# Optimization experiments

Hardware: AMD Instinct MI355X
Metric: run time of the kernel (lower is better)

## Reference

```python
import jax, jax.numpy as jnp
import numpy as np

C = 256          # in_channels
CI = 128         # inter_channels = C // reduction
N_B, H, W = 4, 64, 64


def setup_inputs() -> dict:
    key = jax.random.key(0)
    ks = jax.random.split(key, 9)
    std = 0.01
    inp = {
        "x": jax.random.normal(ks[0], (N_B, C, H, W), dtype=jnp.float32),
        # 1x1 conv weights stored as [out_ch, in_ch]
        "w_g": jax.random.normal(ks[1], (CI, C), dtype=jnp.float32) * std,
        "b_g": jnp.zeros((CI,), dtype=jnp.float32),
        "w_theta": jax.random.normal(ks[2], (CI, C), dtype=jnp.float32) * std,
        "b_theta": jnp.zeros((CI,), dtype=jnp.float32),
        "w_phi": jax.random.normal(ks[3], (CI, C), dtype=jnp.float32) * std,
        "b_phi": jnp.zeros((CI,), dtype=jnp.float32),
        # conv_out: use small random instead of exact zeros so output is non-trivial
        "w_out": jax.random.normal(ks[4], (C, CI), dtype=jnp.float32) * std,
        "b_out": jnp.zeros((C,), dtype=jnp.float32),
    }
    return inp


def reference(x, w_g, b_g, w_theta, b_theta, w_phi, b_phi, w_out, b_out):
    n, c, h, w = x.shape
    nhw = h * w
    xf = x.reshape(n, c, nhw)                                   # [n, C, N]
    # 1x1 convs == channel matmuls
    g_x = jnp.einsum('ncs,oc->nso', xf, w_g) + b_g              # [n, N, CI]
    theta_x = jnp.einsum('ncs,oc->nso', xf, w_theta) + b_theta  # [n, N, CI]
    phi_x = jnp.einsum('ncs,oc->nos', xf, w_phi) + b_phi[None, :, None]  # [n, CI, N]
    # pairwise weights: [n, N, N]
    pw = jnp.einsum('nqc,ncs->nqs', theta_x, phi_x)
    # faithful to original: DIVIDE by d**-0.5 (i.e. multiply by sqrt(d))
    pw = pw / (theta_x.shape[-1] ** (-0.5))
    pw = jax.nn.softmax(pw, axis=-1)
    y = jnp.einsum('nqs,nsc->nqc', pw, g_x)                     # [n, N, CI]
    y = y.transpose(0, 2, 1).reshape(n, -1, h, w)               # [n, CI, H, W]
    out = jnp.einsum('nchw,oc->nohw', y, w_out) + b_out[None, :, None, None]
    return x + out
```

## Files before the change

kernel.cpp:

```cpp
#include <hip/hip_runtime.h>
#include <cmath>

typedef __attribute__((ext_vector_type(8))) short bf16x8;
typedef __attribute__((ext_vector_type(4))) float f32x4;

#define MFMA16(a,b,c) __builtin_amdgcn_mfma_f32_16x16x32_bf16((a),(b),(c),0,0,0)

#if __has_builtin(__builtin_amdgcn_exp2f)
#define EXP2F(x) __builtin_amdgcn_exp2f(x)
#else
#define EXP2F(x) exp2f(x)
#endif

#define KSCALE 16.3222312f
#define SMAX 44.0f

#define NB 4
#define CH 256
#define CI 128
#define NS 4096

__device__ __forceinline__ unsigned short f2bf(float f) {
    unsigned int u = __builtin_bit_cast(unsigned int, f);
    u += 0x7fffu + ((u >> 16) & 1u);
    return (unsigned short)(u >> 16);
}
__device__ __forceinline__ unsigned int pk2(float lo, float hi) {
    return (unsigned int)f2bf(lo) | ((unsigned int)f2bf(hi) << 16);
}
__device__ __forceinline__ unsigned int pk2t(float lo, float hi) {
    unsigned int ul = __builtin_bit_cast(unsigned int, lo);
    unsigned int uh = __builtin_bit_cast(unsigned int, hi);
    return (uh & 0xffff0000u) | (ul >> 16);
}

__device__ __forceinline__ void gload16(void* lds, const void* g) {
    __builtin_amdgcn_global_load_lds(
        (const __attribute__((address_space(1))) unsigned int*)g,
        (__attribute__((address_space(3))) unsigned int*)lds,
        16, 0, 0);
}

__global__ void wcvt_kernel(const float* __restrict__ w_g, const float* __restrict__ w_th,
                            const float* __restrict__ w_ph, const float* __restrict__ w_out,
                            const float* __restrict__ b_g, const float* __restrict__ b_th,
                            const float* __restrict__ b_ph,
                            unsigned short* __restrict__ wbf, float* __restrict__ bsc) {
    int i = blockIdx.x * 256 + threadIdx.x;
    float v;
    if (i < 32768)        v = w_g[i];
    else if (i < 65536)   v = w_th[i - 32768] * KSCALE;
    else if (i < 98304)   v = w_ph[i - 65536];
    else                  v = w_out[i - 98304];
    wbf[i] = f2bf(v);
    if (i < 128)          bsc[i] = b_g[i];
    else if (i < 256)     bsc[i] = b_th[i - 128] * KSCALE;
    else if (i < 384)     bsc[i] = b_ph[i - 256];
}

__global__ __launch_bounds__(256, 2)
void proj_kernel(const float* __restrict__ x,
                 const unsigned short* __restrict__ wbf, const float* __restrict__ bsc,
                 unsigned short* __restrict__ theta,
                 unsigned short* __restrict__ phi,
                 unsigned short* __restrict__ gT) {
    const int tid  = threadIdx.x;
    const int wid  = tid >> 6;
    const int lane = tid & 63;
    const int quad = lane >> 4;
    const int l15  = lane & 15;
    const int wi    = blockIdx.x;
    const int stile = blockIdx.y;
    const int n     = blockIdx.z;
    const int s0    = stile * 128;

    const float* xN = x + (size_t)n * CH * NS;
    const unsigned short* W = wbf + (size_t)wi * 32768;
    const float* Bv = bsc + wi * 128;

    __shared__ unsigned int xp[128 * 68];

    f32x4 acc[8][2];
#pragma unroll
    for (int ot = 0; ot < 8; ot++)
#pragma unroll
        for (int st = 0; st < 2; st++) acc[ot][st] = (f32x4){0.f, 0.f, 0.f, 0.f};

    for (int ch = 0; ch < 2; ch++) {
        __syncthreads();
#pragma unroll
        for (int i = 0; i < 8; i++) {
            int t  = tid + 256 * i;
            int cp = t >> 5;
            int s4 = t & 31;
            int c0 = ch * 128 + cp * 2;
            const float* p0 = xN + (size_t)c0 * NS + s0 + s4 * 4;
            float4 a = *(const float4*)p0;
            float4 b = *(const float4*)(p0 + NS);
            xp[(s4 * 4 + 0) * 68 + cp] = pk2(a.x, b.x);
            xp[(s4 * 4 + 1) * 68 + cp] = pk2(a.y, b.y);
            xp[(s4 * 4 + 2) * 68 + cp] = pk2(a.z, b.z);
            xp[(s4 * 4 + 3) * 68 + cp] = pk2(a.w, b.w);
        }
        __syncthreads();
#pragma unroll
        for (int kc = 0; kc < 4; kc++) {
            bf16x8 af[2];
#pragma unroll
            for (int st = 0; st < 2; st++) {
                int row = wid * 32 + st * 16 + l15;
                af[st] = *(const bf16x8*)(&xp[row * 68 + kc * 16 + quad * 4]);
            }
#pragma unroll
            for (int ot = 0; ot < 8; ot++) {
                bf16x8 bf = *(const bf16x8*)(W + (size_t)(ot * 16 + l15) * CH + ch * 128 + kc * 32 + quad * 8);
#pragma unroll
                for (int st = 0; st < 2; st++)
                    acc[ot][st] = MFMA16(af[st], bf, acc[ot][st]);
            }
        }
    }
#pragma unroll
    for (int ot = 0; ot < 8; ot++) {
        int o = ot * 16 + l15;
        float bias = Bv[o];
#pragma unroll
        for (int st = 0; st < 2; st++) {
#pragma unroll
            for (int r = 0; r < 4; r++) {
                int sg = s0 + wid * 32 + st * 16 + quad * 4 + r;
                float v = acc[ot][st][r] + bias;
                if (wi == 0)
                    gT[((size_t)n * CI + o) * NS + sg] = f2bf(v);
                else if (wi == 1)
                    theta[((size_t)n * NS + sg) * CI + o] = f2bf(v);
                else
                    phi[((size_t)n * NS + sg) * CI + o] = f2bf(v);
            }
        }
    }
}

__global__ __launch_bounds__(512, 2)
void attn_kernel(const unsigned short* __restrict__ theta,
                 const unsigned short* __restrict__ phi,
                 const unsigned short* __restrict__ gT,
                 float* __restrict__ Opart,
                 float* __restrict__ lbuf) {
    const int tid  = threadIdx.x;
    const int wid  = tid >> 6;
    const int lane = tid & 63;
    const int quad = lane >> 4;
    const int l15  = lane & 15;
    const int sn    = blockIdx.x;
    const int split = sn >> 2;
    const int n     = sn & 3;
    const int qb    = blockIdx.y;
    const int qbase = qb * 256 + wid * 32;

    const unsigned short* thN = theta + (size_t)n * NS * CI;
    const unsigned short* phN = phi   + (size_t)n * NS * CI;
    const unsigned short* gN  = gT    + (size_t)n * CI * NS;

    __shared__ unsigned short smem[49152];
    unsigned short* Kb = smem;
    unsigned short* Vb = smem + 16384;
    unsigned short* Plds = smem + 32768;

    bf16x8 qf[2][4];
#pragma unroll
    for (int qt = 0; qt < 2; qt++)
#pragma unroll
        for (int kc = 0; kc < 4; kc++)
            qf[qt][kc] = *(const bf16x8*)(thN + (size_t)(qbase + qt * 16 + l15) * CI + kc * 32 + quad * 8);

    f32x4 O[8][2];
#pragma unroll
    for (int ct = 0; ct < 8; ct++)
#pragma unroll
        for (int qt = 0; qt < 2; qt++) O[ct][qt] = (f32x4){0.f, 0.f, 0.f, 0.f};
    float lrun[2] = {0.f, 0.f};

    const int sbase0 = split * 1024;
    const int lh16 = lane >> 4, lm16 = lane & 15;
    const int lh8  = lane >> 3, lm8  = lane & 7;

#pragma unroll
    for (int i = 0; i < 2; i++) {
        int seg = wid * 2 + i;
        int s   = seg * 4 + lh16;
        int j   = lm16 ^ (s & 15);
        gload16(Kb + seg * 512, phN + (size_t)(sbase0 + s) * CI + j * 8);
    }
#pragma unroll
    for (int i = 0; i < 2; i++) {
        int seg = wid * 2 + i;
        int c   = seg * 8 + lh8;
        int j   = lm8 ^ (c & 7);
        gload16(Vb + seg * 512, gN + (size_t)c * NS + sbase0 + j * 8);
    }

    for (int ck = 0; ck < 16; ck++) {
        const int cur = ck & 1, nxt = cur ^ 1;
        unsigned short* Kc = Kb + cur * 8192;
        unsigned short* Vc = Vb + cur * 8192;
        __syncthreads();

        if (ck + 1 < 16) {
            const int sb1 = sbase0 + (ck + 1) * 64;
#pragma unroll
            for (int i = 0; i < 2; i++) {
                int seg = wid * 2 + i;
                int s   = seg * 4 + lh16;
                int j   = lm16 ^ (s & 15);
                gload16(Kb + nxt * 8192 + seg * 512, phN + (size_t)(sb1 + s) * CI + j * 8);
            }
#pragma unroll
            for (int i = 0; i < 2; i++) {
                int seg = wid * 2 + i;
                int c   = seg * 8 + lh8;
                int j   = lm8 ^ (c & 7);
                gload16(Vb + nxt * 8192 + seg * 512, gN + (size_t)c * NS + sb1 + j * 8);
            }
        }

        f32x4 S[2][4];
#pragma unroll
        for (int qt = 0; qt < 2; qt++)
#pragma unroll
            for (int st = 0; st < 4; st++) S[qt][st] = (f32x4){0.f, 0.f, 0.f, 0.f};
#pragma unroll
        for (int st = 0; st < 4; st++) {
#pragma unroll
            for (int kc = 0; kc < 4; kc++) {
                int s = st * 16 + l15;
                bf16x8 kf = *(const bf16x8*)(Kc + s * 128 + ((kc * 4 + quad) ^ l15) * 8);
#pragma unroll
                for (int qt = 0; qt < 2; qt++)
                    S[qt][st] = MFMA16(kf, qf[qt][kc], S[qt][st]);
            }
        }

#pragma unroll
        for (int qt = 0; qt < 2; qt++) {
            float rsl = 0.f;
            unsigned int u[8];
#pragma unroll
            for (int st = 0; st < 4; st++) {
                float p0 = EXP2F(S[qt][st][0] - SMAX);
                float p1 = EXP2F(S[qt][st][1] - SMAX);
                float p2 = EXP2F(S[qt][st][2] - SMAX);
                float p3 = EXP2F(S[qt][st][3] - SMAX);
                rsl += (p0 + p1) + (p2 + p3);
                u[st * 2]     = pk2t(p0, p1);
                u[st * 2 + 1] = pk2t(p2, p3);
            }
            lrun[qt] += rsl;
            unsigned short* Pw = Plds + (wid * 2 + qt) * 1024 + l15 * 64 + (quad & 1) * 4;
#pragma unroll
            for (int st = 0; st < 4; st++) {
                int p = ((st * 2 + (quad >> 1)) ^ (l15 & 7)) * 8;
                *(uint2*)(Pw + p) = make_uint2(u[st * 2], u[st * 2 + 1]);
            }
        }

#pragma unroll
        for (int kc2 = 0; kc2 < 2; kc2++) {
            bf16x8 pf[2];
#pragma unroll
            for (int qt = 0; qt < 2; qt++)
                pf[qt] = *(const bf16x8*)(Plds + (wid * 2 + qt) * 1024 + l15 * 64 + (((kc2 * 4 + quad) ^ (l15 & 7)) * 8));
#pragma unroll
            for (int ct = 0; ct < 8; ct++) {
                int c = ct * 16 + l15;
                bf16x8 vf = *(const bf16x8*)(Vc + c * 64 + (((kc2 * 4 + quad) ^ (l15 & 7)) * 8));
#pragma unroll
                for (int qt = 0; qt < 2; qt++)
                    O[ct][qt] = MFMA16(vf, pf[qt], O[ct][qt]);
            }
        }
    }

    __syncthreads();
    float* tb = (float*)smem + wid * 2048;
    const size_t obase = ((size_t)(split * NB + n)) * NS * CI;
#pragma unroll
    for (int qt = 0; qt < 2; qt++) {
#pragma unroll
        for (int ct = 0; ct < 8; ct++) {
            int p = (ct * 4 + quad) ^ l15;
            *(f32x4*)(tb + l15 * 128 + p * 4) = O[ct][qt];
        }
#pragma unroll
        for (int i = 0; i < 8; i++) {
            int flat = i * 64 + lane;
            int row = flat >> 5, jj = flat & 31;
            int p2 = jj ^ row;
            f32x4 v = *(const f32x4*)(tb + row * 128 + p2 * 4);
            int q = qbase + qt * 16 + row;
            *(f32x4*)(Opart + obase + (size_t)q * CI + jj * 4) = v;
        }
    }
    lrun[0] += __shfl_xor(lrun[0], 16); lrun[0] += __shfl_xor(lrun[0], 32);
    lrun[1] += __shfl_xor(lrun[1], 16); lrun[1] += __shfl_xor(lrun[1], 32);
    if (quad == 0) {
#pragma unroll
        for (int qt = 0; qt < 2; qt++) {
            int q = qbase + qt * 16 + l15;
            lbuf[split * (NB * NS) + n * NS + q] = lrun[qt];
        }
    }
}

__global__ __launch_bounds__(256, 2)
void outproj_kernel(const float* __restrict__ x,
                    const unsigned short* __restrict__ wbf,
                    const float* __restrict__ b_out,
                    const float* __restrict__ Opart,
                    const float* __restrict__ lbuf,
                    float* __restrict__ out) {
    const int tid  = threadIdx.x;
    const int wid  = tid >> 6;
    const int lane = tid & 63;
    const int quad = lane >> 4;
    const int l15  = lane & 15;
    const int oh = blockIdx.y;
    const int n  = blockIdx.z;
    const int sw = blockIdx.x * 64 + wid * 16;
    const int T  = NB * NS;

    const int srow = n * NS + sw + l15;
    float l = lbuf[srow] + lbuf[T + srow] + lbuf[2 * T + srow] + lbuf[3 * T + srow];
    float rinv = 1.0f / l;

    bf16x8 yb[4];
#pragma unroll
    for (int kc = 0; kc < 4; kc++) {
        float a0 = 0.f, a1 = 0.f, a2 = 0.f, a3 = 0.f;
        float b0 = 0.f, b1 = 0.f, b2 = 0.f, b3 = 0.f;
#pragma unroll
        for (int k = 0; k < 4; k++) {
            const float* p = Opart + ((size_t)k * T + srow) * CI + kc * 32 + quad * 8;
            float4 u = *(const float4*)p;
            float4 v = *(const float4*)(p + 4);
            a0 += u.x; a1 += u.y; a2 += u.z; a3 += u.w;
            b0 += v.x; b1 += v.y; b2 += v.z; b3 += v.w;
        }
        union { unsigned int uu[4]; bf16x8 vv; } r;
        r.uu[0] = pk2(a0 * rinv, a1 * rinv);
        r.uu[1] = pk2(a2 * rinv, a3 * rinv);
        r.uu[2] = pk2(b0 * rinv, b1 * rinv);
        r.uu[3] = pk2(b2 * rinv, b3 * rinv);
        yb[kc] = r.vv;
    }

    const unsigned short* wob = wbf + 3 * 32768 + (size_t)oh * 128 * CI;
    f32x4 acc[8];
#pragma unroll
    for (int ot = 0; ot < 8; ot++) acc[ot] = (f32x4){0.f, 0.f, 0.f, 0.f};
#pragma unroll
    for (int kc = 0; kc < 4; kc++) {
#pragma unroll
        for (int ot = 0; ot < 8; ot++) {
            bf16x8 wa = *(const bf16x8*)(wob + (size_t)(ot * 16 + l15) * CI + kc * 32 + quad * 8);
            acc[ot] = MFMA16(wa, yb[kc], acc[ot]);
        }
    }
#pragma unroll
    for (int ot = 0; ot < 8; ot++) {
#pragma unroll
        for (int r = 0; r < 4; r++) {
            int o = oh * 128 + ot * 16 + quad * 4 + r;
            size_t idx = ((size_t)n * CH + o) * NS + sw + l15;
            out[idx] = x[idx] + acc[ot][r] + b_out[o];
        }
    }
}

extern "C" void kernel_launch(void* const* d_in, const int* in_sizes, int n_in,
                              void* d_out, int out_size, void* d_ws, size_t ws_size,
                              hipStream_t stream) {
    const float* x     = (const float*)d_in[0];
    const float* w_g   = (const float*)d_in[1];
    const float* b_g   = (const float*)d_in[2];
    const float* w_th  = (const float*)d_in[3];
    const float* b_th  = (const float*)d_in[4];
    const float* w_ph  = (const float*)d_in[5];
    const float* b_ph  = (const float*)d_in[6];
    const float* w_out = (const float*)d_in[7];
    const float* b_out = (const float*)d_in[8];
    float* out = (float*)d_out;

    char* ws = (char*)d_ws;
    unsigned short* theta = (unsigned short*)(ws + 0);
    unsigned short* phi   = (unsigned short*)(ws + 4194304);
    unsigned short* gT    = (unsigned short*)(ws + 8388608);
    float* Opart = (float*)(ws + 12582912);
    float* lbuf  = (float*)(ws + 46137344);
    unsigned short* wbf = (unsigned short*)(ws + 50855936);
    float* bsc   = (float*)(ws + 51118080);

    wcvt_kernel<<<512, 256, 0, stream>>>(w_g, w_th, w_ph, w_out, b_g, b_th, b_ph, wbf, bsc);
    proj_kernel<<<dim3(3, 32, NB), 256, 0, stream>>>(x, wbf, bsc, theta, phi, gT);
    attn_kernel<<<dim3(16, 16), 512, 0, stream>>>(theta, phi, gT, Opart, lbuf);
    outproj_kernel<<<dim3(64, 2, NB), 256, 0, stream>>>(x, wbf, b_out, Opart, lbuf, out);
}
```

Measured before the change: 168.5 us.

## Restructure attention into 8 key splits with 64-query warps and bf16 partials

The attention kernel goes from 512-thread blocks with 4 key splits of 1024 and 32 queries per warp to 256-thread blocks with 8 splits of 512 and 64 queries per warp. The key/value chunk shrinks to 32 keys, so per-chunk LDS is halved and each K/V fragment loaded from LDS feeds four query tiles instead of two. Partial outputs are stored as bf16 instead of fp32, halving the partial-sum write and read traffic, and the output projection now sums 8 partials. Costs are more registers per thread, twice as many partial rows to reduce, and added bf16 rounding error in the partial outputs.

```diff
diff --git a/kernel.cpp b/kernel.cpp
--- a/kernel.cpp
+++ b/kernel.cpp
@@ -32,6 +32,9 @@
     unsigned int ul = __builtin_bit_cast(unsigned int, lo);
     unsigned int uh = __builtin_bit_cast(unsigned int, hi);
     return (uh & 0xffff0000u) | (ul >> 16);
+}
+__device__ __forceinline__ float bf2f(unsigned int ush) {
+    return __builtin_bit_cast(float, ush << 16);
 }
 
 __device__ __forceinline__ void gload16(void* lds, const void* g) {
@@ -141,11 +144,11 @@
     }
 }
 
-__global__ __launch_bounds__(512, 2)
+__global__ __launch_bounds__(256, 2)
 void attn_kernel(const unsigned short* __restrict__ theta,
                  const unsigned short* __restrict__ phi,
                  const unsigned short* __restrict__ gT,
-                 float* __restrict__ Opart,
+                 unsigned short* __restrict__ Opart,
                  float* __restrict__ lbuf) {
     const int tid  = threadIdx.x;
     const int wid  = tid >> 6;
@@ -156,34 +159,34 @@
     const int split = sn >> 2;
     const int n     = sn & 3;
     const int qb    = blockIdx.y;
-    const int qbase = qb * 256 + wid * 32;
+    const int qbase = qb * 256 + wid * 64;
 
     const unsigned short* thN = theta + (size_t)n * NS * CI;
     const unsigned short* phN = phi   + (size_t)n * NS * CI;
     const unsigned short* gN  = gT    + (size_t)n * CI * NS;
 
-    __shared__ unsigned short smem[49152];
+    __shared__ unsigned short smem[24576];
     unsigned short* Kb = smem;
-    unsigned short* Vb = smem + 16384;
-    unsigned short* Plds = smem + 32768;
-
-    bf16x8 qf[2][4];
-#pragma unroll
-    for (int qt = 0; qt < 2; qt++)
+    unsigned short* Vb = smem + 8192;
+    unsigned short* Plds = smem + 16384;
+
+    bf16x8 qf[4][4];
+#pragma unroll
+    for (int qt = 0; qt < 4; qt++)
 #pragma unroll
         for (int kc = 0; kc < 4; kc++)
             qf[qt][kc] = *(const bf16x8*)(thN + (size_t)(qbase + qt * 16 + l15) * CI + kc * 32 + quad * 8);
 
-    f32x4 O[8][2];
+    f32x4 O[8][4];
 #pragma unroll
     for (int ct = 0; ct < 8; ct++)
 #pragma unroll
-        for (int qt = 0; qt < 2; qt++) O[ct][qt] = (f32x4){0.f, 0.f, 0.f, 0.f};
-    float lrun[2] = {0.f, 0.f};
-
-    const int sbase0 = split * 1024;
+        for (int qt = 0; qt < 4; qt++) O[ct][qt] = (f32x4){0.f, 0.f, 0.f, 0.f};
+    float lrun[4] = {0.f, 0.f, 0.f, 0.f};
+
+    const int sbase0 = split * 512;
     const int lh16 = lane >> 4, lm16 = lane & 15;
-    const int lh8  = lane >> 3, lm8  = lane & 7;
+    const int lh4  = lane >> 2, lm4  = lane & 3;
 
 #pragma unroll
     for (int i = 0; i < 2; i++) {
@@ -195,89 +198,71 @@
 #pragma unroll
     for (int i = 0; i < 2; i++) {
         int seg = wid * 2 + i;
-        int c   = seg * 8 + lh8;
-        int j   = lm8 ^ (c & 7);
+        int c   = seg * 16 + lh4;
+        int j   = lm4 ^ (c & 3);
         gload16(Vb + seg * 512, gN + (size_t)c * NS + sbase0 + j * 8);
     }
 
     for (int ck = 0; ck < 16; ck++) {
         const int cur = ck & 1, nxt = cur ^ 1;
-        unsigned short* Kc = Kb + cur * 8192;
-        unsigned short* Vc = Vb + cur * 8192;
+        unsigned short* Kc = Kb + cur * 4096;
+        unsigned short* Vc = Vb + cur * 4096;
         __syncthreads();
 
         if (ck + 1 < 16) {
-            const int sb1 = sbase0 + (ck + 1) * 64;
+            const int sb1 = sbase0 + (ck + 1) * 32;
 #pragma unroll
             for (int i = 0; i < 2; i++) {
                 int seg = wid * 2 + i;
                 int s   = seg * 4 + lh16;
                 int j   = lm16 ^ (s & 15);
-                gload16(Kb + nxt * 8192 + seg * 512, phN + (size_t)(sb1 + s) * CI + j * 8);
+                gload16(Kb + nxt * 4096 + seg * 512, phN + (size_t)(sb1 + s) * CI + j * 8);
             }
 #pragma unroll
             for (int i = 0; i < 2; i++) {
                 int seg = wid * 2 + i;
-                int c   = seg * 8 + lh8;
-                int j   = lm8 ^ (c & 7);
-                gload16(Vb + nxt * 8192 + seg * 512, gN + (size_t)c * NS + sb1 + j * 8);
-            }
-        }
-
-        f32x4 S[2][4];
-#pragma unroll
-        for (int qt = 0; qt < 2; qt++)
-#pragma unroll
-            for (int st = 0; st < 4; st++) S[qt][st] = (f32x4){0.f, 0.f, 0.f, 0.f};
-#pragma unroll
-        for (int st = 0; st < 4; st++) {
+                int c   = seg * 16 + lh4;
+                int j   = lm4 ^ (c & 3);
+                gload16(Vb + nxt * 4096 + seg * 512, gN + (size_t)c * NS + sb1 + j * 8);
+            }
+        }
+
+#pragma unroll
+        for (int st = 0; st < 2; st++) {
+            f32x4 S[4];
+#pragma unroll
+            for (int qt = 0; qt < 4; qt++) S[qt] = (f32x4){0.f, 0.f, 0.f, 0.f};
 #pragma unroll
             for (int kc = 0; kc < 4; kc++) {
-                int s = st * 16 + l15;
-                bf16x8 kf = *(const bf16x8*)(Kc + s * 128 + ((kc * 4 + quad) ^ l15) * 8);
-#pragma unroll
-                for (int qt = 0; qt < 2; qt++)
-                    S[qt][st] = MFMA16(kf, qf[qt][kc], S[qt][st]);
-            }
-        }
-
-#pragma unroll
-        for (int qt = 0; qt < 2; qt++) {
-            float rsl = 0.f;
-            unsigned int u[8];
-#pragma unroll
-            for (int st = 0; st < 4; st++) {
-                float p0 = EXP2F(S[qt][st][0] - SMAX);
-                float p1 = EXP2F(S[qt][st][1] - SMAX);
-                float p2 = EXP2F(S[qt][st][2] - SMAX);
-                float p3 = EXP2F(S[qt][st][3] - SMAX);
-                rsl += (p0 + p1) + (p2 + p3);
-                u[st * 2]     = pk2t(p0, p1);
-                u[st * 2 + 1] = pk2t(p2, p3);
-            }
-            lrun[qt] += rsl;
-            unsigned short* Pw = Plds + (wid * 2 + qt) * 1024 + l15 * 64 + (quad & 1) * 4;
-#pragma unroll
-            for (int st = 0; st < 4; st++) {
-                int p = ((st * 2 + (quad >> 1)) ^ (l15 & 7)) * 8;
-                *(uint2*)(Pw + p) = make_uint2(u[st * 2], u[st * 2 + 1]);
-            }
-        }
-
-#pragma unroll
-        for (int kc2 = 0; kc2 < 2; kc2++) {
-            bf16x8 pf[2];
-#pragma unroll
-            for (int qt = 0; qt < 2; qt++)
-                pf[qt] = *(const bf16x8*)(Plds + (wid * 2 + qt) * 1024 + l15 * 64 + (((kc2 * 4 + quad) ^ (l15 & 7)) * 8));
-#pragma unroll
-            for (int ct = 0; ct < 8; ct++) {
-                int c = ct * 16 + l15;
-                bf16x8 vf = *(const bf16x8*)(Vc + c * 64 + (((kc2 * 4 + quad) ^ (l15 & 7)) * 8));
-#pragma unroll
-                for (int qt = 0; qt < 2; qt++)
-                    O[ct][qt] = MFMA16(vf, pf[qt], O[ct][qt]);
-            }
+                bf16x8 kf = *(const bf16x8*)(Kc + (st * 16 + l15) * 128 + ((kc * 4 + quad) ^ l15) * 8);
+#pragma unroll
+                for (int qt = 0; qt < 4; qt++)
+                    S[qt] = MFMA16(kf, qf[qt][kc], S[qt]);
+            }
+#pragma unroll
+            for (int qt = 0; qt < 4; qt++) {
+                float p0 = EXP2F(S[qt][0] - SMAX);
+                float p1 = EXP2F(S[qt][1] - SMAX);
+                float p2 = EXP2F(S[qt][2] - SMAX);
+                float p3 = EXP2F(S[qt][3] - SMAX);
+                lrun[qt] += (p0 + p1) + (p2 + p3);
+                unsigned short* Pw = Plds + wid * 2048 + qt * 512 + l15 * 32;
+                int cidx = (st * 2 + (quad >> 1)) ^ (l15 & 3);
+                *(uint2*)(Pw + cidx * 8 + (quad & 1) * 4) =
+                    make_uint2(pk2t(p0, p1), pk2t(p2, p3));
+            }
+        }
+
+        bf16x8 pf[4];
+#pragma unroll
+        for (int qt = 0; qt < 4; qt++)
+            pf[qt] = *(const bf16x8*)(Plds + wid * 2048 + qt * 512 + l15 * 32 + (quad ^ (l15 & 3)) * 8);
+#pragma unroll
+        for (int ct = 0; ct < 8; ct++) {
+            bf16x8 vf = *(const bf16x8*)(Vc + (ct * 16 + l15) * 32 + (quad ^ (l15 & 3)) * 8);
+#pragma unroll
+            for (int qt = 0; qt < 4; qt++)
+                O[ct][qt] = MFMA16(vf, pf[qt], O[ct][qt]);
         }
     }
 
@@ -285,38 +270,44 @@
     float* tb = (float*)smem + wid * 2048;
     const size_t obase = ((size_t)(split * NB + n)) * NS * CI;
 #pragma unroll
-    for (int qt = 0; qt < 2; qt++) {
+    for (int qt = 0; qt < 4; qt++) {
 #pragma unroll
         for (int ct = 0; ct < 8; ct++) {
             int p = (ct * 4 + quad) ^ l15;
             *(f32x4*)(tb + l15 * 128 + p * 4) = O[ct][qt];
         }
 #pragma unroll
-        for (int i = 0; i < 8; i++) {
+        for (int i = 0; i < 4; i++) {
             int flat = i * 64 + lane;
-            int row = flat >> 5, jj = flat & 31;
-            int p2 = jj ^ row;
-            f32x4 v = *(const f32x4*)(tb + row * 128 + p2 * 4);
+            int row = flat >> 4, jj = flat & 15;
+            f32x4 a = *(const f32x4*)(tb + row * 128 + ((jj * 2) ^ row) * 4);
+            f32x4 b = *(const f32x4*)(tb + row * 128 + ((jj * 2 + 1) ^ row) * 4);
             int q = qbase + qt * 16 + row;
-            *(f32x4*)(Opart + obase + (size_t)q * CI + jj * 4) = v;
-        }
-    }
-    lrun[0] += __shfl_xor(lrun[0], 16); lrun[0] += __shfl_xor(lrun[0], 32);
-    lrun[1] += __shfl_xor(lrun[1], 16); lrun[1] += __shfl_xor(lrun[1], 32);
+            uint4 pkv;
+            pkv.x = pk2(a[0], a[1]); pkv.y = pk2(a[2], a[3]);
+            pkv.z = pk2(b[0], b[1]); pkv.w = pk2(b[2], b[3]);
+            *(uint4*)(Opart + obase + (size_t)q * CI + jj * 8) = pkv;
+        }
+    }
+#pragma unroll
+    for (int qt = 0; qt < 4; qt++) {
+        lrun[qt] += __shfl_xor(lrun[qt], 16);
+        lrun[qt] += __shfl_xor(lrun[qt], 32);
+    }
     if (quad == 0) {
 #pragma unroll
-        for (int qt = 0; qt < 2; qt++) {
+        for (int qt = 0; qt < 4; qt++) {
             int q = qbase + qt * 16 + l15;
-            lbuf[split * (NB * NS) + n * NS + q] = lrun[qt];
-        }
-    }
-}
-
-__global__ __launch_bounds__(256, 2)
+            lbuf[(split * NB + n) * NS + q] = lrun[qt];
+        }
+    }
+}
+
+__global__ __launch_bounds__(256, 4)
 void outproj_kernel(const float* __restrict__ x,
                     const unsigned short* __restrict__ wbf,
                     const float* __restrict__ b_out,
-                    const float* __restrict__ Opart,
+                    const unsigned short* __restrict__ Opart,
                     const float* __restrict__ lbuf,
                     float* __restrict__ out) {
     const int tid  = threadIdx.x;
@@ -330,27 +321,29 @@
     const int T  = NB * NS;
 
     const int srow = n * NS + sw + l15;
-    float l = lbuf[srow] + lbuf[T + srow] + lbuf[2 * T + srow] + lbuf[3 * T + srow];
+    float l = 0.f;
+#pragma unroll
+    for (int k = 0; k < 8; k++) l += lbuf[k * T + srow];
     float rinv = 1.0f / l;
 
     bf16x8 yb[4];
 #pragma unroll
     for (int kc = 0; kc < 4; kc++) {
-        float a0 = 0.f, a1 = 0.f, a2 = 0.f, a3 = 0.f;
-        float b0 = 0.f, b1 = 0.f, b2 = 0.f, b3 = 0.f;
-#pragma unroll
-        for (int k = 0; k < 4; k++) {
-            const float* p = Opart + ((size_t)k * T + srow) * CI + kc * 32 + quad * 8;
-            float4 u = *(const float4*)p;
-            float4 v = *(const float4*)(p + 4);
-            a0 += u.x; a1 += u.y; a2 += u.z; a3 += u.w;
-            b0 += v.x; b1 += v.y; b2 += v.z; b3 += v.w;
+        float f0 = 0.f, f1 = 0.f, f2 = 0.f, f3 = 0.f;
+        float f4 = 0.f, f5 = 0.f, f6 = 0.f, f7 = 0.f;
+#pragma unroll
+        for (int k = 0; k < 8; k++) {
+            uint4 v = *(const uint4*)(Opart + ((size_t)k * T + srow) * CI + kc * 32 + quad * 8);
+            f0 += bf2f(v.x & 0xffffu); f1 += bf2f(v.x >> 16);
+            f2 += bf2f(v.y & 0xffffu); f3 += bf2f(v.y >> 16);
+            f4 += bf2f(v.z & 0xffffu); f5 += bf2f(v.z >> 16);
+            f6 += bf2f(v.w & 0xffffu); f7 += bf2f(v.w >> 16);
         }
         union { unsigned int uu[4]; bf16x8 vv; } r;
-        r.uu[0] = pk2(a0 * rinv, a1 * rinv);
-        r.uu[1] = pk2(a2 * rinv, a3 * rinv);
-        r.uu[2] = pk2(b0 * rinv, b1 * rinv);
-        r.uu[3] = pk2(b2 * rinv, b3 * rinv);
+        r.uu[0] = pk2(f0 * rinv, f1 * rinv);
+        r.uu[1] = pk2(f2 * rinv, f3 * rinv);
+        r.uu[2] = pk2(f4 * rinv, f5 * rinv);
+        r.uu[3] = pk2(f6 * rinv, f7 * rinv);
         yb[kc] = r.vv;
     }
 
@@ -395,13 +388,13 @@
     unsigned short* theta = (unsigned short*)(ws + 0);
     unsigned short* phi   = (unsigned short*)(ws + 4194304);
     unsigned short* gT    = (unsigned short*)(ws + 8388608);
-    float* Opart = (float*)(ws + 12582912);
+    unsigned short* Opart = (unsigned short*)(ws + 12582912);
     float* lbuf  = (float*)(ws + 46137344);
     unsigned short* wbf = (unsigned short*)(ws + 50855936);
     float* bsc   = (float*)(ws + 51118080);
 
     wcvt_kernel<<<512, 256, 0, stream>>>(w_g, w_th, w_ph, w_out, b_g, b_th, b_ph, wbf, bsc);
     proj_kernel<<<dim3(3, 32, NB), 256, 0, stream>>>(x, wbf, bsc, theta, phi, gT);
-    attn_kernel<<<dim3(16, 16), 512, 0, stream>>>(theta, phi, gT, Opart, lbuf);
+    attn_kernel<<<dim3(32, 16), 256, 0, stream>>>(theta, phi, gT, Opart, lbuf);
     outproj_kernel<<<dim3(64, 2, NB), 256, 0, stream>>>(x, wbf, b_out, Opart, lbuf, out);
 }
```

New measurement: 190.6 us. 13.1% more time.
